# Performance work log

Measured on AMD Instinct MI355X. Metric: run time of the kernel, lower is better.

The kernel has to match this reference:

```python
import jax, jax.numpy as jnp
import numpy as np

SEQ, BATCH, HIDDEN = 2048, 2, 2048
NUM_HEADS = 16
HEAD_DIM = HIDDEN // NUM_HEADS  # 128


def setup_inputs() -> dict:
    key = jax.random.key(0)
    k1, k2, k3, k4, k5 = jax.random.split(key, 5)
    scale = 1.0 / np.sqrt(HIDDEN)
    return {
        "hidden_states": jax.random.normal(k1, (SEQ, BATCH, HIDDEN), dtype=jnp.float32),
        "w_qkv": jax.random.normal(k2, (3 * HIDDEN, HIDDEN), dtype=jnp.float32) * scale,
        "b_qkv": jax.random.normal(k3, (3 * HIDDEN,), dtype=jnp.float32) * 0.01,
        "w_dense": jax.random.normal(k4, (HIDDEN, HIDDEN), dtype=jnp.float32) * scale,
        "b_dense": jax.random.normal(k5, (HIDDEN,), dtype=jnp.float32) * 0.01,
    }


def reference(hidden_states, w_qkv, b_qkv, w_dense, b_dense):
    s, b, H = hidden_states.shape
    nh, d = NUM_HEADS, HEAD_DIM
    norm_factor = jnp.asarray(np.sqrt(d), dtype=hidden_states.dtype)

    # QKV projection: [s, b, 3H] -> [s, b, nh, 3d] -> chunk into q, k, v
    mixed = hidden_states @ w_qkv.T + b_qkv
    mixed = mixed.reshape(s, b, nh, 3 * d)
    q, k, v = jnp.split(mixed, 3, axis=-1)  # each [s, b, nh, d]

    # Causal scaled dot-product attention, materializing [b, nh, sq, sk]
    scores = jnp.einsum("sbhd,tbhd->bhst", q, k) / norm_factor
    causal = jnp.tril(jnp.ones((s, s), dtype=bool))  # [sq, sk]
    scores = jnp.where(causal[None, None, :, :], scores, jnp.asarray(-10000.0, scores.dtype))
    probs = jax.nn.softmax(scores, axis=-1)

    # Context: [s, b, nh, d] -> [s, b, H]
    ctx = jnp.einsum("bhst,tbhd->sbhd", probs, v).reshape(s, b, H)

    # Output projection
    return ctx @ w_dense.T + b_dense
```

## Files before the change

kernel.cpp:

```cpp
#include <hip/hip_runtime.h>
#include <stdint.h>
#include <stddef.h>

#define SEQ   2048
#define BATCH 2
#define HID   2048
#define NH    16
#define HD    128
#define MTOT  (SEQ*BATCH)
#define NQKV  (3*HID)
#define KDIM  HID
#define LOG2E 1.4426950408889634f

#define BK64    64
#define NT64    (KDIM/BK64)

typedef short  bf16x8 __attribute__((ext_vector_type(8)));
typedef float  f32x4  __attribute__((ext_vector_type(4)));

__device__ __forceinline__ unsigned short f2bf(float f) {
  union { float f; uint32_t u; } a; a.f = f;
  uint32_t r = a.u + 0x7fffu + ((a.u >> 16) & 1u);
  return (unsigned short)(r >> 16);
}

__device__ __forceinline__ f32x4 mfma16(bf16x8 a, bf16x8 b, f32x4 c) {
  return __builtin_amdgcn_mfma_f32_16x16x32_bf16(a, b, c, 0, 0, 0);
}

__device__ __forceinline__ void gl_lds16(const unsigned short* g, unsigned short* l) {
  __builtin_amdgcn_global_load_lds(
      (const __attribute__((address_space(1))) void*)g,
      (__attribute__((address_space(3))) void*)l, 16, 0, 0);
}

__global__ void cvt_f32_bf16(const float* __restrict__ in,
                             unsigned short* __restrict__ out, int n4) {
  int i = blockIdx.x * blockDim.x + threadIdx.x;
  int stride = gridDim.x * blockDim.x;
  for (; i < n4; i += stride) {
    float4 f = reinterpret_cast<const float4*>(in)[i];
    ushort4 o;
    o.x = f2bf(f.x); o.y = f2bf(f.y); o.z = f2bf(f.z); o.w = f2bf(f.w);
    reinterpret_cast<ushort4*>(out)[i] = o;
  }
}

__global__ __launch_bounds__(256) void transpose_v(
    const unsigned short* __restrict__ V, unsigned short* __restrict__ Vt) {
  __shared__ unsigned short tile[64][72];
  const int t  = threadIdx.x;
  const int bh = blockIdx.z;
  const int s0 = blockIdx.x * 64;
  const int d0 = blockIdx.y * 64;
  const size_t vb = (size_t)bh * SEQ * HD;
  const size_t tb = (size_t)bh * HD * SEQ;
#pragma unroll
  for (int p = 0; p < 2; ++p) {
    int r = p * 32 + (t >> 3);
    *(uint4*)&tile[r][(t & 7) * 8] =
        *(const uint4*)&V[vb + (size_t)(s0 + r) * HD + d0 + (t & 7) * 8];
  }
  __syncthreads();
#pragma unroll
  for (int p = 0; p < 2; ++p) {
    int dr = p * 32 + (t >> 3);
    int sc = (t & 7) * 8;
    unsigned short tmp[8];
#pragma unroll
    for (int e = 0; e < 8; ++e) tmp[e] = tile[sc + e][dr];
    *(uint4*)&Vt[tb + (size_t)(d0 + dr) * SEQ + s0 + sc] = *(const uint4*)tmp;
  }
}


#define GEMM_PRE()                                                            \
  const int t = threadIdx.x, l = t & 63, w = t >> 6;                          \
  const int wm = w >> 1, wn = w & 1;                                          \
  const int fr = l & 15, fg = l >> 4;                                         \
  const int fx = fr & 7;                                                      \
  const int srow = l >> 3;                                                    \
  const int sgr  = ((l & 7) ^ srow) * 8;                                      \
  const unsigned short* Aw = A + (size_t)(m0 + w * 32 + srow) * KDIM + sgr;   \
  const unsigned short* Bw = B + (size_t)(n0 + w * 16 + srow) * KDIM + sgr;   \
  unsigned short* smb = &sm[0][0];                                            \
  const int a0 = (wm * 64 + fr) * 64 + ((fg ^ fx) * 8);                       \
  const int a1 = (wm * 64 + fr) * 64 + (((4 + fg) ^ fx) * 8);                 \
  const int b0 = 16384 + (wn * 64 + fr) * 64 + ((fg ^ fx) * 8);               \
  const int b1 = 16384 + (wn * 64 + fr) * 64 + (((4 + fg) ^ fx) * 8);         \
  f32x4 acc[4][4] = {};

#define STAGE_AB(KT) do {                                                     \
    unsigned short* dst = &smb[((KT) % 3) * 24576];                           \
    const unsigned short* ap = Aw + (size_t)(KT) * BK64;                      \
    gl_lds16(ap,                    &dst[(w * 4 + 0) * 512]);                 \
    gl_lds16(ap + 8  * KDIM,        &dst[(w * 4 + 1) * 512]);                 \
    gl_lds16(ap + 16 * KDIM,        &dst[(w * 4 + 2) * 512]);                 \
    gl_lds16(ap + 24 * KDIM,        &dst[(w * 4 + 3) * 512]);                 \
    const unsigned short* bp = Bw + (size_t)(KT) * BK64;                      \
    gl_lds16(bp,                    &dst[16384 + (w * 2 + 0) * 512]);         \
    gl_lds16(bp + 8 * KDIM,         &dst[16384 + (w * 2 + 1) * 512]);         \
  } while (0)

#define GEMM_BODY(KT, VM, DOSTAGE) do {                                       \
    const unsigned short* sb = &smb[((KT) % 3) * 24576];                      \
    if (DOSTAGE) STAGE_AB((KT) + 2);                                          \
    bf16x8 af0[4], af1[4], bg0[4], bg1[4];                                    \
    _Pragma("unroll")                                                         \
    for (int m_ = 0; m_ < 4; ++m_) {                                          \
      af0[m_] = *(const bf16x8*)&sb[a0 + m_ * 1024];                          \
      af1[m_] = *(const bf16x8*)&sb[a1 + m_ * 1024];                          \
    }                                                                         \
    _Pragma("unroll")                                                         \
    for (int n_ = 0; n_ < 4; ++n_) {                                          \
      bg0[n_] = *(const bf16x8*)&sb[b0 + n_ * 1024];                          \
      bg1[n_] = *(const bf16x8*)&sb[b1 + n_ * 1024];                          \
    }                                                                         \
    asm volatile("s_waitcnt vmcnt(" #VM ")" ::: "memory");                    \
    asm volatile("s_barrier" ::: "memory");                                   \
    asm volatile("s_waitcnt lgkmcnt(0)" ::: "memory");                        \
    __builtin_amdgcn_sched_barrier(0);                                        \
    __builtin_amdgcn_s_setprio(1);                                            \
    _Pragma("unroll")                                                         \
    for (int m_ = 0; m_ < 4; ++m_)                                            \
      _Pragma("unroll")                                                       \
      for (int n_ = 0; n_ < 4; ++n_)                                          \
        acc[m_][n_] = mfma16(af0[m_], bg0[n_], acc[m_][n_]);                  \
    _Pragma("unroll")                                                         \
    for (int m_ = 0; m_ < 4; ++m_)                                            \
      _Pragma("unroll")                                                       \
      for (int n_ = 0; n_ < 4; ++n_)                                          \
        acc[m_][n_] = mfma16(af1[m_], bg1[n_], acc[m_][n_]);                  \
    __builtin_amdgcn_sched_barrier(0);                                        \
    __builtin_amdgcn_s_setprio(0);                                            \
    asm volatile("s_barrier" ::: "memory");                                   \
  } while (0)

#define GEMM_MAIN()                                                           \
  STAGE_AB(0); STAGE_AB(1);                                                   \
  asm volatile("s_waitcnt vmcnt(6)" ::: "memory");                            \
  asm volatile("s_barrier" ::: "memory");                                     \
  _Pragma("unroll 1")                                                         \
  for (int kt = 0; kt < NT64 - 2; ++kt)                                       \
    GEMM_BODY(kt, 6, 1);                                                      \
  GEMM_BODY(NT64 - 2, 0, 0);                                                  \
  GEMM_BODY(NT64 - 1, 0, 0);

__global__ __launch_bounds__(512, 1) void qkv_gemm(
    const unsigned short* __restrict__ A,
    const unsigned short* __restrict__ B,
    const float* __restrict__ bias,
    unsigned short* __restrict__ Qo,
    unsigned short* __restrict__ Ko,
    unsigned short* __restrict__ Vo)
{
  __shared__ unsigned short sm[3][24576];
  int id  = blockIdx.x;
  int swz = (id & 7) * (gridDim.x >> 3) + (id >> 3);
  const int m0 = (swz / 48) * 256, n0 = (swz % 48) * 128;
  GEMM_PRE();
  GEMM_MAIN();

  const int g4 = fg * 4;
#pragma unroll
  for (int n = 0; n < 4; ++n) {
    int ncol = n0 + wn * 64 + n * 16 + fr;
    float bv = bias[ncol];
    int head = ncol / 384;
    int rem  = ncol - head * 384;
    int wi   = rem >> 7;
    int d    = rem & 127;
    unsigned short* dst = (wi == 0) ? Qo : ((wi == 1) ? Ko : Vo);
#pragma unroll
    for (int m = 0; m < 4; ++m) {
#pragma unroll
      for (int j = 0; j < 4; ++j) {
        int r = m0 + wm * 64 + m * 16 + g4 + j;
        int s = r >> 1, bb = r & 1;
        float val = acc[m][n][j] + bv;
        if (wi == 0) val *= 0.08838834764831845f;
        dst[(((size_t)(bb * NH + head)) * SEQ + s) * HD + d] = f2bf(val);
      }
    }
  }
}

__global__ __launch_bounds__(512, 1) void dense_gemm(
    const unsigned short* __restrict__ A,
    const unsigned short* __restrict__ B,
    const float* __restrict__ bias,
    float* __restrict__ out)
{
  __shared__ unsigned short sm[3][24576];
  int id  = blockIdx.x;
  int swz = (id & 7) * (gridDim.x >> 3) + (id >> 3);
  const int m0 = (swz / 16) * 256, n0 = (swz % 16) * 128;
  GEMM_PRE();
  GEMM_MAIN();

  const int g4 = fg * 4;
#pragma unroll
  for (int n = 0; n < 4; ++n) {
    int ncol = n0 + wn * 64 + n * 16 + fr;
    float bv = bias[ncol];
#pragma unroll
    for (int m = 0; m < 4; ++m) {
#pragma unroll
      for (int j = 0; j < 4; ++j) {
        int r = m0 + wm * 64 + m * 16 + g4 + j;
        out[(size_t)r * HID + ncol] = acc[m][n][j] + bv;
      }
    }
  }
}

__global__ __launch_bounds__(256, 2) void attn_fwd(
    const unsigned short* __restrict__ Q,
    const unsigned short* __restrict__ K,
    const unsigned short* __restrict__ Vt,
    unsigned short* __restrict__ ctx)
{
  __shared__ unsigned short Ksh[2][64 * 128];
  __shared__ unsigned short Vsh[2][128 * 64];
  __shared__ unsigned short Psh[4][16 * 72];
  const int t = threadIdx.x, l = t & 63, w = t >> 6;
  int nwg = gridDim.x * gridDim.y;
  int id  = blockIdx.y * gridDim.x + blockIdx.x;
  int swz = (id & 7) * (nwg >> 3) + (id >> 3);
  const int pair = swz & 15;
  const int bh   = swz >> 4;
  const int qtA = pair, qtB = 31 - pair;
  const int fr = l & 15, fg = l >> 4;
  const size_t base  = (size_t)bh * SEQ * HD;
  const size_t vbase = (size_t)bh * HD * SEQ;

#define STAGE(BUF, KT) do {                                                   \
    const unsigned short* Kt_ = K + base + (size_t)((KT) * 64) * HD;          \
    _Pragma("unroll")                                                         \
    for (int i_ = 0; i_ < 4; ++i_) {                                          \
      int ch_  = w * 4 + i_;                                                  \
      int row_ = ch_ * 4 + (l >> 4);                                          \
      int c16_ = (l & 15) ^ (row_ & 7);                                       \
      gl_lds16(Kt_ + (size_t)row_ * HD + c16_ * 8, &Ksh[BUF][ch_ * 512]);     \
    }                                                                         \
    const unsigned short* Vg_ = Vt + vbase + (KT) * 64;                       \
    _Pragma("unroll")                                                         \
    for (int i_ = 0; i_ < 4; ++i_) {                                          \
      int ch_  = w * 4 + i_;                                                  \
      int row_ = ch_ * 8 + (l >> 3);                                          \
      int c16_ = (l & 7) ^ (row_ & 7);                                        \
      gl_lds16(Vg_ + (size_t)row_ * SEQ + c16_ * 8, &Vsh[BUF][ch_ * 512]);    \
    }                                                                         \
  } while (0)

#define COMPUTE_TILE(QF, OACC, MROW, LROW, QT) do {                           \
    f32x4 sacc[4] = {};                                                       \
    _Pragma("unroll")                                                         \
    for (int c_ = 0; c_ < 4; ++c_) {                                          \
      _Pragma("unroll")                                                       \
      for (int n_ = 0; n_ < 4; ++n_) {                                        \
        int krow = n_ * 16 + fr;                                              \
        int g_   = (c_ * 4 + fg) ^ (krow & 7);                                \
        bf16x8 kf = *(const bf16x8*)&Ksh[buf][krow * 128 + g_ * 8];           \
        sacc[n_] = mfma16(QF[c_], kf, sacc[n_]);                              \
      }                                                                       \
    }                                                                         \
    if (kt == (QT)) {                                                         \
      _Pragma("unroll")                                                       \
      for (int n_ = 0; n_ < 4; ++n_)                                          \
        _Pragma("unroll")                                                     \
        for (int j_ = 0; j_ < 4; ++j_)                                        \
          if (n_ * 16 + fr > w * 16 + fg * 4 + j_) sacc[n_][j_] = -1e30f;     \
    }                                                                         \
    float tm_[4];                                                             \
    _Pragma("unroll")                                                         \
    for (int j_ = 0; j_ < 4; ++j_) {                                          \
      float v0 = fmaxf(fmaxf(sacc[0][j_], sacc[1][j_]),                       \
                       fmaxf(sacc[2][j_], sacc[3][j_]));                      \
      v0 = fmaxf(v0, __shfl_xor(v0, 1));                                      \
      v0 = fmaxf(v0, __shfl_xor(v0, 2));                                      \
      v0 = fmaxf(v0, __shfl_xor(v0, 4));                                      \
      v0 = fmaxf(v0, __shfl_xor(v0, 8));                                      \
      tm_[j_] = v0;                                                           \
    }                                                                         \
    float sc_[4], ps_[4];                                                     \
    _Pragma("unroll")                                                         \
    for (int j_ = 0; j_ < 4; ++j_) {                                          \
      float mn_ = fmaxf(MROW[j_], tm_[j_]);                                   \
      sc_[j_] = exp2f((MROW[j_] - mn_) * LOG2E);                              \
      MROW[j_] = mn_;                                                         \
      ps_[j_] = 0.f;                                                          \
    }                                                                         \
    _Pragma("unroll")                                                         \
    for (int n_ = 0; n_ < 4; ++n_)                                            \
      _Pragma("unroll")                                                       \
      for (int j_ = 0; j_ < 4; ++j_) {                                        \
        float p_ = exp2f((sacc[n_][j_] - MROW[j_]) * LOG2E);                  \
        sacc[n_][j_] = p_;                                                    \
        ps_[j_] += p_;                                                        \
      }                                                                       \
    _Pragma("unroll")                                                         \
    for (int j_ = 0; j_ < 4; ++j_) {                                          \
      float s_ = ps_[j_];                                                     \
      s_ += __shfl_xor(s_, 1);                                                \
      s_ += __shfl_xor(s_, 2);                                                \
      s_ += __shfl_xor(s_, 4);                                                \
      s_ += __shfl_xor(s_, 8);                                                \
      LROW[j_] = LROW[j_] * sc_[j_] + s_;                                     \
    }                                                                         \
    _Pragma("unroll")                                                         \
    for (int n_ = 0; n_ < 8; ++n_)                                            \
      _Pragma("unroll")                                                       \
      for (int j_ = 0; j_ < 4; ++j_)                                          \
        OACC[n_][j_] *= sc_[j_];                                              \
    _Pragma("unroll")                                                         \
    for (int n_ = 0; n_ < 4; ++n_)                                            \
      _Pragma("unroll")                                                       \
      for (int j_ = 0; j_ < 4; ++j_)                                          \
        Psh[w][(fg * 4 + j_) * 72 + n_ * 16 + fr] = f2bf(sacc[n_][j_]);       \
    _Pragma("unroll")                                                         \
    for (int ks_ = 0; ks_ < 2; ++ks_) {                                       \
      bf16x8 pf = *(const bf16x8*)&Psh[w][fr * 72 + ks_ * 32 + fg * 8];       \
      _Pragma("unroll")                                                       \
      for (int n_ = 0; n_ < 8; ++n_) {                                        \
        int vrow = n_ * 16 + fr;                                              \
        int g_   = (ks_ * 4 + fg) ^ (vrow & 7);                               \
        bf16x8 vf = *(const bf16x8*)&Vsh[buf][vrow * 64 + g_ * 8];            \
        OACC[n_] = mfma16(pf, vf, OACC[n_]);                                  \
      }                                                                       \
    }                                                                         \
  } while (0)

  bf16x8 qfA[4], qfB[4];
  {
    const unsigned short* qpA = Q + base + (size_t)(qtA * 64 + w * 16 + fr) * HD + fg * 8;
    const unsigned short* qpB = Q + base + (size_t)(qtB * 64 + w * 16 + fr) * HD + fg * 8;
#pragma unroll
    for (int c = 0; c < 4; ++c) {
      qfA[c] = *(const bf16x8*)(qpA + c * 32);
      qfB[c] = *(const bf16x8*)(qpB + c * 32);
    }
  }
  f32x4 oaccA[8] = {}, oaccB[8] = {};
  float mA[4] = {-1e30f, -1e30f, -1e30f, -1e30f};
  float mB[4] = {-1e30f, -1e30f, -1e30f, -1e30f};
  float lA[4] = {0.f, 0.f, 0.f, 0.f};
  float lB[4] = {0.f, 0.f, 0.f, 0.f};

  STAGE(0, 0);
  __syncthreads();
  int buf = 0;
  for (int kt = 0; kt <= qtB; ++kt) {
    if (kt < qtB) STAGE(buf ^ 1, kt + 1);
    COMPUTE_TILE(qfB, oaccB, mB, lB, qtB);
    if (kt <= qtA) COMPUTE_TILE(qfA, oaccA, mA, lA, qtA);
    __syncthreads();
    buf ^= 1;
  }

  const int bb = bh >> 4, h = bh & 15;
#define WRITE_CTX(OACC, LROW, QT) do {                                        \
    _Pragma("unroll")                                                         \
    for (int n_ = 0; n_ < 8; ++n_)                                            \
      _Pragma("unroll")                                                       \
      for (int j_ = 0; j_ < 4; ++j_) {                                        \
        int qrow = (QT) * 64 + w * 16 + fg * 4 + j_;                          \
        float val = OACC[n_][j_] / LROW[j_];                                  \
        ctx[((size_t)(qrow * BATCH + bb)) * HID + h * HD + n_ * 16 + fr] =    \
            f2bf(val);                                                        \
      }                                                                       \
  } while (0)
  WRITE_CTX(oaccA, lA, qtA);
  WRITE_CTX(oaccB, lB, qtB);
#undef STAGE
#undef COMPUTE_TILE
#undef WRITE_CTX
}

extern "C" void kernel_launch(void* const* d_in, const int* in_sizes, int n_in,
                              void* d_out, int out_size, void* d_ws, size_t ws_size,
                              hipStream_t stream) {
  const float* hs      = (const float*)d_in[0];
  const float* w_qkv   = (const float*)d_in[1];
  const float* b_qkv   = (const float*)d_in[2];
  const float* w_dense = (const float*)d_in[3];
  const float* b_dense = (const float*)d_in[4];
  float* out = (float*)d_out;

  unsigned short* hsb = (unsigned short*)d_ws;
  unsigned short* wqb = hsb + (size_t)MTOT * HID;
  unsigned short* wdb = wqb + (size_t)NQKV * HID;
  unsigned short* q   = wdb + (size_t)HID * HID;
  unsigned short* k   = q   + (size_t)MTOT * HID;
  unsigned short* v   = k   + (size_t)MTOT * HID;
  unsigned short* ctx = v   + (size_t)MTOT * HID;
  unsigned short* vt  = hsb;

  cvt_f32_bf16<<<2048, 256, 0, stream>>>(hs,      hsb, (MTOT * HID) / 4);
  cvt_f32_bf16<<<2048, 256, 0, stream>>>(w_qkv,   wqb, (NQKV * HID) / 4);
  cvt_f32_bf16<<<1024, 256, 0, stream>>>(w_dense, wdb, (HID * HID) / 4);

  qkv_gemm<<<dim3((MTOT / 256) * (NQKV / 128)), 512, 0, stream>>>(hsb, wqb, b_qkv, q, k, v);
  transpose_v<<<dim3(SEQ / 64, HD / 64, BATCH * NH), 256, 0, stream>>>(v, vt);
  attn_fwd<<<dim3(16, 32), 256, 0, stream>>>(q, k, vt, ctx);
  dense_gemm<<<dim3((MTOT / 256) * (HID / 128)), 512, 0, stream>>>(ctx, wdb, b_dense, out);
}
```

Baseline: 274.7 us.

## Rewrite QKV GEMM with 256x256 tiles and 8-wave interleaved double buffering

Replaces the 256x128-tile QKV projection kernel with a 256x256-tile version. The new version uses 8 waves in a 2x4 layout and a two-buffer LDS pipeline. Each K-step is split into four phases that interleave global-to-LDS loads with MFMA groups under barriers and priority hints. The larger tile is meant to raise arithmetic intensity and halve the redundant operand loads. The cost is 128 accumulator registers per thread and a 128 KB LDS footprint, and the grid shrinks to 384 blocks.

```diff
diff --git a/kernel.cpp b/kernel.cpp
--- a/kernel.cpp
+++ b/kernel.cpp
@@ -70,6 +70,142 @@
 #pragma unroll
     for (int e = 0; e < 8; ++e) tmp[e] = tile[sc + e][dr];
     *(uint4*)&Vt[tb + (size_t)(d0 + dr) * SEQ + s0 + sc] = *(const uint4*)tmp;
+  }
+}
+
+
+#define G8_SB()  asm volatile("s_barrier" ::: "memory")
+#define G8_LGKM() do { asm volatile("s_waitcnt lgkmcnt(0)" ::: "memory");     \
+                       __builtin_amdgcn_sched_barrier(0); } while (0)
+
+#define G8_RDA(G) do {                                                        \
+    p0 = *(const bf16x8*)&sb[abase + (2*(G)    ) * 1024 + ga0];               \
+    p1 = *(const bf16x8*)&sb[abase + (2*(G)    ) * 1024 + ga1];               \
+    p2 = *(const bf16x8*)&sb[abase + (2*(G) + 1) * 1024 + ga0];               \
+    p3 = *(const bf16x8*)&sb[abase + (2*(G) + 1) * 1024 + ga1];               \
+  } while (0)
+
+#define G8_MFMA(G) do {                                                       \
+    __builtin_amdgcn_s_setprio(1);                                            \
+    _Pragma("unroll")                                                         \
+    for (int n_ = 0; n_ < 4; ++n_) {                                          \
+      acc[2*(G)][n_]     = mfma16(p0, bq0[n_], acc[2*(G)][n_]);               \
+      acc[2*(G)][n_]     = mfma16(p1, bq1[n_], acc[2*(G)][n_]);               \
+      acc[2*(G) + 1][n_] = mfma16(p2, bq0[n_], acc[2*(G) + 1][n_]);           \
+      acc[2*(G) + 1][n_] = mfma16(p3, bq1[n_], acc[2*(G) + 1][n_]);           \
+    }                                                                         \
+    __builtin_amdgcn_sched_barrier(0);                                        \
+    __builtin_amdgcn_s_setprio(0);                                            \
+  } while (0)
+
+#define G8_STA(R) gl_lds16(Asrc + (size_t)(R) * KDIM + koff,                  \
+                           &db[((R) + w * 8) * 64])
+#define G8_STB(R) gl_lds16(Bsrc + (size_t)(R) * KDIM + koff,                  \
+                           &db[16384 + ((R) + w * 8) * 64])
+
+#define G8_TILE(DOSTAGE, VM1, VM3) do {                                       \
+    bf16x8 bq0[4], bq1[4], p0, p1, p2, p3;                                    \
+                                                       \
+    _Pragma("unroll")                                                         \
+    for (int n_ = 0; n_ < 4; ++n_) {                                          \
+      bq0[n_] = *(const bf16x8*)&sb[bbase + n_ * 1024 + ga0];                 \
+      bq1[n_] = *(const bf16x8*)&sb[bbase + n_ * 1024 + ga1];                 \
+    }                                                                         \
+    G8_RDA(0);                                                                \
+    if (DOSTAGE) { G8_STB(0); G8_STB(64); }                                   \
+    G8_SB(); G8_LGKM();                                                       \
+    G8_MFMA(0);                                                               \
+    G8_SB();                                                                  \
+                                                       \
+    G8_RDA(1);                                                                \
+    if (DOSTAGE) { G8_STB(128); G8_STB(192); }                                \
+    asm volatile("s_waitcnt " VM1 ::: "memory");                              \
+    G8_SB(); G8_LGKM();                                                       \
+    G8_MFMA(1);                                                               \
+    G8_SB();                                                                  \
+                                                       \
+    G8_RDA(2);                                                                \
+    if (DOSTAGE) { G8_STA(0); G8_STA(128); }                                  \
+    G8_SB(); G8_LGKM();                                                       \
+    G8_MFMA(2);                                                               \
+    G8_SB();                                                                  \
+                                                       \
+    G8_RDA(3);                                                                \
+    if (DOSTAGE) { G8_STA(64); G8_STA(192); }                                 \
+    asm volatile("s_waitcnt " VM3 ::: "memory");                              \
+    G8_SB(); G8_LGKM();                                                       \
+    G8_MFMA(3);                                                               \
+    G8_SB();                                                                  \
+  } while (0)
+
+__global__ __launch_bounds__(512, 2) void qkv_gemm(
+    const unsigned short* __restrict__ A,
+    const unsigned short* __restrict__ B,
+    const float* __restrict__ bias,
+    unsigned short* __restrict__ Qo,
+    unsigned short* __restrict__ Ko,
+    unsigned short* __restrict__ Vo)
+{
+  __shared__ unsigned short smb[2 * 32768];
+  const int id  = blockIdx.x;
+  const int swz = (id & 7) * 48 + (id >> 3);
+  const int m0 = (swz / 24) * 256, n0 = (swz % 24) * 256;
+  const int t = threadIdx.x, l = t & 63, w = t >> 6;
+  const int wm = w >> 2, wn = w & 3;
+  const int fr = l & 15, fg = l >> 4;
+  const int abase = (wm * 128 + fr) * 64;
+  const int bbase = 16384 + (wn * 64 + fr) * 64;
+  const int ga0 = ((fg     ) ^ (fr & 7)) * 8;
+  const int ga1 = ((fg + 4 ) ^ (fr & 7)) * 8;
+  const int srcrow = w * 8 + (l >> 3);
+  const int sgr    = ((l & 7) ^ (l >> 3)) * 8;
+  const unsigned short* Asrc = A + (size_t)(m0 + srcrow) * KDIM + sgr;
+  const unsigned short* Bsrc = B + (size_t)(n0 + srcrow) * KDIM + sgr;
+  f32x4 acc[8][4] = {};
+
+  {
+    unsigned short* db = smb;
+    size_t koff = 0;
+    G8_STB(0); G8_STB(64); G8_STB(128); G8_STB(192);
+    G8_STA(0); G8_STA(128); G8_STA(64); G8_STA(192);
+  }
+  asm volatile("s_waitcnt vmcnt(2)" ::: "memory");
+  asm volatile("s_barrier" ::: "memory");
+
+#pragma unroll 1
+  for (int kt = 0; kt < NT64 - 1; ++kt) {
+    const unsigned short* sb = &smb[(kt & 1) * 32768];
+    unsigned short* db = &smb[((kt + 1) & 1) * 32768];
+    size_t koff = (size_t)(kt + 1) * BK64;
+    G8_TILE(1, "vmcnt(4)", "vmcnt(2)");
+  }
+  {
+    const unsigned short* sb = &smb[((NT64 - 1) & 1) * 32768];
+    unsigned short* db = smb;
+    size_t koff = 0; (void)koff;
+    G8_TILE(0, "vmcnt(0)", "vmcnt(0)");
+  }
+
+#pragma unroll
+  for (int n = 0; n < 4; ++n) {
+    int ncol = n0 + wn * 64 + n * 16 + fr;
+    float bv = bias[ncol];
+    int head = ncol / 384;
+    int rem  = ncol - head * 384;
+    int wi   = rem >> 7;
+    int d    = rem & 127;
+    unsigned short* dst = (wi == 0) ? Qo : ((wi == 1) ? Ko : Vo);
+#pragma unroll
+    for (int m = 0; m < 8; ++m) {
+#pragma unroll
+      for (int j = 0; j < 4; ++j) {
+        int r = m0 + wm * 128 + m * 16 + fg * 4 + j;
+        int s = r >> 1, bb = r & 1;
+        float val = acc[m][n][j] + bv;
+        if (wi == 0) val *= 0.08838834764831845f;
+        dst[(((size_t)(bb * NH + head)) * SEQ + s) * HD + d] = f2bf(val);
+      }
+    }
   }
 }
 
@@ -145,45 +281,6 @@
     GEMM_BODY(kt, 6, 1);                                                      \
   GEMM_BODY(NT64 - 2, 0, 0);                                                  \
   GEMM_BODY(NT64 - 1, 0, 0);
-
-__global__ __launch_bounds__(512, 1) void qkv_gemm(
-    const unsigned short* __restrict__ A,
-    const unsigned short* __restrict__ B,
-    const float* __restrict__ bias,
-    unsigned short* __restrict__ Qo,
-    unsigned short* __restrict__ Ko,
-    unsigned short* __restrict__ Vo)
-{
-  __shared__ unsigned short sm[3][24576];
-  int id  = blockIdx.x;
-  int swz = (id & 7) * (gridDim.x >> 3) + (id >> 3);
-  const int m0 = (swz / 48) * 256, n0 = (swz % 48) * 128;
-  GEMM_PRE();
-  GEMM_MAIN();
-
-  const int g4 = fg * 4;
-#pragma unroll
-  for (int n = 0; n < 4; ++n) {
-    int ncol = n0 + wn * 64 + n * 16 + fr;
-    float bv = bias[ncol];
-    int head = ncol / 384;
-    int rem  = ncol - head * 384;
-    int wi   = rem >> 7;
-    int d    = rem & 127;
-    unsigned short* dst = (wi == 0) ? Qo : ((wi == 1) ? Ko : Vo);
-#pragma unroll
-    for (int m = 0; m < 4; ++m) {
-#pragma unroll
-      for (int j = 0; j < 4; ++j) {
-        int r = m0 + wm * 64 + m * 16 + g4 + j;
-        int s = r >> 1, bb = r & 1;
-        float val = acc[m][n][j] + bv;
-        if (wi == 0) val *= 0.08838834764831845f;
-        dst[(((size_t)(bb * NH + head)) * SEQ + s) * HD + d] = f2bf(val);
-      }
-    }
-  }
-}
 
 __global__ __launch_bounds__(512, 1) void dense_gemm(
     const unsigned short* __restrict__ A,
@@ -400,7 +497,7 @@
   cvt_f32_bf16<<<2048, 256, 0, stream>>>(w_qkv,   wqb, (NQKV * HID) / 4);
   cvt_f32_bf16<<<1024, 256, 0, stream>>>(w_dense, wdb, (HID * HID) / 4);
 
-  qkv_gemm<<<dim3((MTOT / 256) * (NQKV / 128)), 512, 0, stream>>>(hsb, wqb, b_qkv, q, k, v);
+  qkv_gemm<<<dim3((MTOT / 256) * (NQKV / 256)), 512, 0, stream>>>(hsb, wqb, b_qkv, q, k, v);
   transpose_v<<<dim3(SEQ / 64, HD / 64, BATCH * NH), 256, 0, stream>>>(v, vt);
   attn_fwd<<<dim3(16, 32), 256, 0, stream>>>(q, k, vt, ctx);
   dense_gemm<<<dim3((MTOT / 256) * (HID / 128)), 512, 0, stream>>>(ctx, wdb, b_dense, out);
```

Result: slower. 285.4 us (+3.9%).
